# Optimization experiments

Measured on AMD Instinct MI355X. Metric: run time of the kernel, lower is better.

## Reference

```python
import jax, jax.numpy as jnp
import numpy as np

B, S, E, H = 8, 2048, 1024, 128  # batch, seq, emd_dim, head_size
DROP_P = 0.1


def setup_inputs() -> dict:
    key = jax.random.key(0)
    kx, ku, kq, kk, kv = jax.random.split(key, 5)
    x = jax.random.normal(kx, (B, S, E), dtype=jnp.float32)
    drop_u = jax.random.uniform(ku, (B, S, S), dtype=jnp.float32)
    # Linear(emd_dim, head_size, bias=False): store weights as [E, H] so y = x @ W
    scale = 1.0 / np.sqrt(E)
    wq = jax.random.uniform(kq, (E, H), dtype=jnp.float32, minval=-scale, maxval=scale)
    wk = jax.random.uniform(kk, (E, H), dtype=jnp.float32, minval=-scale, maxval=scale)
    wv = jax.random.uniform(kv, (E, H), dtype=jnp.float32, minval=-scale, maxval=scale)
    return {"x": x, "wq": wq, "wk": wk, "wv": wv, "drop_u": drop_u}


def reference(x, wq, wk, wv, drop_u):
    Edim = x.shape[-1]
    q = x @ wq  # [B,S,H]
    k = x @ wk
    v = x @ wv
    # NOTE: module scales by emd_dim**-0.5 (E), not head_size**-0.5
    att = jnp.einsum("bsh,bth->bst", q, k) * (Edim ** -0.5)
    att = jax.nn.softmax(att, axis=-1)
    # deterministic inverted dropout with p=0.1
    keep = (drop_u >= DROP_P).astype(att.dtype) / (1.0 - DROP_P)
    att = att * keep
    return jnp.einsum("bst,bth->bsh", att, v)
```

## Files before the change

kernel.cpp:

```cpp
#include <hip/hip_runtime.h>
#include <hip/hip_bf16.h>
#include <stdint.h>
#include <stddef.h>

#define B_ 8
#define S_ 2048
#define E_ 1024
#define H_ 128
#define NR_ (B_ * S_)

typedef __attribute__((ext_vector_type(8))) short short8;
typedef __attribute__((ext_vector_type(4))) float f32x4;

__device__ __forceinline__ short f2bf(float f){
  uint32_t u = __builtin_bit_cast(uint32_t, f);
  u = (u + 0x7FFFu + ((u >> 16) & 1u)) >> 16;
  return (short)(uint16_t)u;
}

#define GLOBAL_AS __attribute__((address_space(1)))
#define LDS_AS    __attribute__((address_space(3)))
__device__ __forceinline__ void async16(const void* g, void* l){
  __builtin_amdgcn_global_load_lds((const GLOBAL_AS uint32_t*)g,
                                   (LDS_AS uint32_t*)l, 16, 0, 0);
}

__global__ void pack_w(const float* __restrict__ wq, const float* __restrict__ wk,
                       const float* __restrict__ wv, short* __restrict__ wt){
  __shared__ float t[32][33];
  int idx = blockIdx.x;
  int hb  = idx & 3;
  int eb  = (idx >> 2) & 31;
  int w   = idx >> 7;
  const float* src = (w == 0) ? wq : (w == 1) ? wk : wv;
  int c  = threadIdx.x & 31;
  int r0 = threadIdx.x >> 5;
#pragma unroll
  for (int i = 0; i < 4; i++){
    int r = r0 * 4 + i;
    t[r][c] = src[(size_t)(eb * 32 + r) * H_ + hb * 32 + c];
  }
  __syncthreads();
#pragma unroll
  for (int i = 0; i < 4; i++){
    int r = r0 * 4 + i;
    wt[(size_t)(w * 128 + hb * 32 + r) * E_ + eb * 32 + c] = f2bf(t[c][r]);
  }
}

__launch_bounds__(256)
__global__ void qkv_gemm(const float* __restrict__ x, const short* __restrict__ wt,
                         short* __restrict__ qm, short* __restrict__ km,
                         short* __restrict__ vtmp){
  __shared__ __align__(16) short slab[2][12288];
  const int wave = threadIdx.x >> 6;
  const int lane = threadIdx.x & 63;
  const int l16  = lane & 15;
  const int quad = lane >> 4;
  const int m0   = blockIdx.x * 32;

  f32x4 acc[2][6];
#pragma unroll
  for (int a = 0; a < 2; a++)
#pragma unroll
    for (int b = 0; b < 6; b++) acc[a][b] = (f32x4)(0.0f);

  const float* xr0 = x + (size_t)(m0 + l16) * E_ + quad * 8;
  const float* xr1 = xr0 + (size_t)16 * E_;

#define STAGE(buf, k0)                                                        \
  {                                                                           \
    _Pragma("unroll")                                                         \
    for (int i = 0; i < 6; i++){                                              \
      int c  = wave * 6 + i;                                                  \
      int kc = c & 3;                                                         \
      int nb = c >> 2;                                                        \
      const short* gp = wt + (size_t)(nb * 64 + lane) * E_ + (k0) + kc * 8;   \
      async16(gp, (char*)slab[buf] + kc * 6144 + nb * 1024);                  \
    }                                                                         \
  }

  STAGE(0, 0)
  for (int ks = 0; ks < 32; ks++){
    const int k0 = ks * 32;
    __syncthreads();
    if (ks < 31) STAGE((ks + 1) & 1, k0 + 32)

    f32x4 a00 = *(const f32x4*)(xr0 + k0);
    f32x4 a01 = *(const f32x4*)(xr0 + k0 + 4);
    f32x4 a10 = *(const f32x4*)(xr1 + k0);
    f32x4 a11 = *(const f32x4*)(xr1 + k0 + 4);
    short8 af0, af1;
#pragma unroll
    for (int j = 0; j < 4; j++){
      af0[j] = f2bf(a00[j]); af0[j + 4] = f2bf(a01[j]);
      af1[j] = f2bf(a10[j]); af1[j + 4] = f2bf(a11[j]);
    }

    const char* sb = (const char*)slab[ks & 1];
#pragma unroll
    for (int j = 0; j < 6; j++){
      int nt = wave * 6 + j;
      short8 bf = *(const short8*)(sb + quad * 6144 + (size_t)(nt * 16 + l16) * 16);
      acc[0][j] = __builtin_amdgcn_mfma_f32_16x16x32_bf16(af0, bf, acc[0][j], 0, 0, 0);
      acc[1][j] = __builtin_amdgcn_mfma_f32_16x16x32_bf16(af1, bf, acc[1][j], 0, 0, 0);
    }
  }
#undef STAGE

#pragma unroll
  for (int mt = 0; mt < 2; mt++)
#pragma unroll
    for (int j = 0; j < 6; j++){
      int c0  = wave * 96 + j * 16;
      short* dst = (c0 < 128) ? qm : (c0 < 256) ? km : vtmp;
      int cin = c0 & 127;
      int row = m0 + mt * 16 + quad * 4;
#pragma unroll
      for (int r = 0; r < 4; r++)
        dst[(size_t)(row + r) * H_ + cin + l16] = f2bf(acc[mt][j][r]);
    }
}

__global__ void transpose_v(const short* __restrict__ v, short* __restrict__ vt){
  __shared__ short t[32][33];
  int idx = blockIdx.x;
  int hb = idx & 3;
  int sb = (idx >> 2) & 63;
  int b  = idx >> 8;
  int s0 = sb * 32, h0 = hb * 32;
  int c  = threadIdx.x & 31;
  int r0 = threadIdx.x >> 5;
#pragma unroll
  for (int i = 0; i < 4; i++){
    int r = r0 * 4 + i;
    t[r][c] = v[((size_t)b * S_ + s0 + r) * H_ + h0 + c];
  }
  __syncthreads();
#pragma unroll
  for (int i = 0; i < 4; i++){
    int r = r0 * 4 + i;
    vt[((size_t)b * H_ + h0 + r) * S_ + s0 + c] = t[c][r];
  }
}

__launch_bounds__(256)
__global__ void attn(const short* __restrict__ qm, const short* __restrict__ km,
                     const short* __restrict__ vtm, const float* __restrict__ du,
                     float* __restrict__ po, float* __restrict__ pl,
                     float* __restrict__ out, int split){
  const int wave = threadIdx.x >> 6;
  const int lane = threadIdx.x & 63;
  const int l16  = lane & 15;
  const int quad = lane >> 4;
  const int sp   = blockIdx.x & (split - 1);
  const int rbk  = blockIdx.x / split;
  const int b    = rbk >> 5;
  const int m0   = (rbk & 31) * 64 + wave * 16;
  const int seg  = S_ / split;

  const short* qb  = qm  + ((size_t)b * S_ + m0) * H_;
  const short* kb  = km  + (size_t)b * S_ * H_;
  const short* vb  = vtm + (size_t)b * H_ * S_;
  const float* dub = du  + ((size_t)b * S_ + m0) * S_;

  __shared__ __align__(16) short kls[8192];
  __shared__ __align__(16) short vls[8192];
  __shared__ float pbuf[4][16][68];
  float* pb = &pbuf[wave][0][0];

  short8 qf[4];
#pragma unroll
  for (int kc = 0; kc < 4; kc++)
    qf[kc] = *(const short8*)(qb + (size_t)l16 * H_ + kc * 32 + quad * 8);

  f32x4 o[8];
#pragma unroll
  for (int ht = 0; ht < 8; ht++) o[ht] = (f32x4)(0.0f);
  float lpart[4] = {0.f, 0.f, 0.f, 0.f};

  const float SC2  = 0.045084220f;
  const float KINV = 1.0f / 0.9f;

  const int tbeg = sp * seg;
  for (int t0 = tbeg; t0 < tbeg + seg; t0 += 64){
#pragma unroll
    for (int i = 0; i < 4; i++){
      int c = wave * 4 + i;
      int r = c * 4 + (lane >> 4);
      int s = lane & 15;
      int q = (s & 8) | ((s ^ r) & 7);
      async16(kb + (size_t)(t0 + r) * H_ + q * 8, (char*)kls + c * 1024);
    }
#pragma unroll
    for (int i = 0; i < 4; i++){
      int c = wave * 4 + i;
      int r = c * 8 + (lane >> 3);
      int s = lane & 7;
      int q = (s ^ r) & 7;
      async16(vb + (size_t)r * S_ + t0 + q * 8, (char*)vls + c * 1024);
    }
    __syncthreads();

    const float* dp = dub + (size_t)l16 * S_ + t0 + quad * 8;
    f32x4 u0 = *(const f32x4*)(dp);
    f32x4 u1 = *(const f32x4*)(dp + 4);
    f32x4 u2 = *(const f32x4*)(dp + 32);
    f32x4 u3 = *(const f32x4*)(dp + 36);

    f32x4 s[4];
#pragma unroll
    for (int nt = 0; nt < 4; nt++) s[nt] = (f32x4)(0.0f);
#pragma unroll
    for (int nt = 0; nt < 4; nt++){
      int row = nt * 16 + l16;
#pragma unroll
      for (int kc = 0; kc < 4; kc++){
        int q  = kc * 4 + quad;
        int ph = (q & 8) | ((q ^ row) & 7);
        short8 bf = *(const short8*)((const char*)kls + row * 256 + ph * 16);
        s[nt] = __builtin_amdgcn_mfma_f32_16x16x32_bf16(qf[kc], bf, s[nt], 0, 0, 0);
      }
    }

#pragma unroll
    for (int nt = 0; nt < 4; nt++)
#pragma unroll
      for (int r = 0; r < 4; r++){
        float p = exp2f(s[nt][r] * SC2);
        lpart[r] += p;
        pb[(quad * 4 + r) * 68 + nt * 16 + l16] = p;
      }

    __builtin_amdgcn_sched_barrier(0);
    __builtin_amdgcn_s_waitcnt(0xC07F);
    __builtin_amdgcn_sched_barrier(0);

    const float* pr = pb + l16 * 68 + quad * 8;
    f32x4 p0 = *(const f32x4*)(pr);
    f32x4 p1 = *(const f32x4*)(pr + 4);
    f32x4 p2 = *(const f32x4*)(pr + 32);
    f32x4 p3 = *(const f32x4*)(pr + 36);
    short8 pa0, pa1;
#pragma unroll
    for (int j = 0; j < 4; j++){
      pa0[j]     = f2bf((u0[j] >= 0.1f) ? p0[j] * KINV : 0.0f);
      pa0[j + 4] = f2bf((u1[j] >= 0.1f) ? p1[j] * KINV : 0.0f);
      pa1[j]     = f2bf((u2[j] >= 0.1f) ? p2[j] * KINV : 0.0f);
      pa1[j + 4] = f2bf((u3[j] >= 0.1f) ? p3[j] * KINV : 0.0f);
    }

#pragma unroll
    for (int ht = 0; ht < 8; ht++){
      int row = ht * 16 + l16;
#pragma unroll
      for (int half = 0; half < 2; half++){
        int q  = half * 4 + quad;
        int ph = (q ^ row) & 7;
        short8 vf = *(const short8*)((const char*)vls + row * 128 + ph * 16);
        o[ht] = __builtin_amdgcn_mfma_f32_16x16x32_bf16(half ? pa1 : pa0, vf, o[ht], 0, 0, 0);
      }
    }
    __syncthreads();
  }

  float lrow[4];
#pragma unroll
  for (int r = 0; r < 4; r++){
    float v = lpart[r];
    v += __shfl_xor(v, 1);
    v += __shfl_xor(v, 2);
    v += __shfl_xor(v, 4);
    v += __shfl_xor(v, 8);
    lrow[r] = v;
  }

  if (split == 1){
    float* op = out + ((size_t)b * S_ + m0) * H_;
#pragma unroll
    for (int ht = 0; ht < 8; ht++)
#pragma unroll
      for (int r = 0; r < 4; r++)
        op[(size_t)(quad * 4 + r) * H_ + ht * 16 + l16] = o[ht][r] / lrow[r];
  } else {
#pragma unroll
    for (int r = 0; r < 4; r++){
      size_t R = (size_t)b * S_ + m0 + quad * 4 + r;
#pragma unroll
      for (int ht = 0; ht < 8; ht++)
        po[((size_t)sp * NR_ + R) * H_ + ht * 16 + l16] = o[ht][r];
      if (l16 == 0) pl[(size_t)sp * NR_ + R] = lrow[r];
    }
  }
}

__global__ void combine(const float* __restrict__ po, const float* __restrict__ pl,
                        float* __restrict__ out, int split){
  int row = blockIdx.x;
  int col = threadIdx.x;
  float num = 0.f, den = 0.f;
  for (int s = 0; s < split; s++){
    num += po[((size_t)s * NR_ + row) * H_ + col];
    den += pl[(size_t)s * NR_ + row];
  }
  out[(size_t)row * H_ + col] = num / den;
}

extern "C" void kernel_launch(void* const* d_in, const int* in_sizes, int n_in,
                              void* d_out, int out_size, void* d_ws, size_t ws_size,
                              hipStream_t stream){
  const float* x  = (const float*)d_in[0];
  const float* wq = (const float*)d_in[1];
  const float* wk = (const float*)d_in[2];
  const float* wv = (const float*)d_in[3];
  const float* du = (const float*)d_in[4];
  float* out = (float*)d_out;

  const size_t MiB = 1048576;
  char* ws = (char*)d_ws;
  short* qm  = (short*)(ws);
  short* km  = (short*)(ws + 4 * MiB);
  short* vt  = (short*)(ws + 8 * MiB);
  float* pl  = (float*)(ws + 12 * MiB);
  float* po  = (float*)(ws + 12 * MiB + 524288);
  short* wt   = (short*)(ws + 12 * MiB + 524288);
  short* vtmp = (short*)(ws + 12 * MiB + 524288 + 1 * MiB);

  size_t base  = 12 * MiB + 524288;
  size_t need4 = base + 4 * 8 * MiB;
  size_t need2 = base + 2 * 8 * MiB;
  int split = (ws_size >= need4) ? 4 : (ws_size >= need2) ? 2 : 1;

  hipLaunchKernelGGL(pack_w,      dim3(384),  dim3(256), 0, stream, wq, wk, wv, wt);
  hipLaunchKernelGGL(qkv_gemm,    dim3(512),  dim3(256), 0, stream, x, wt, qm, km, vtmp);
  hipLaunchKernelGGL(transpose_v, dim3(2048), dim3(256), 0, stream, vtmp, vt);
  hipLaunchKernelGGL(attn, dim3(256 * split), dim3(256), 0, stream,
                     qm, km, vt, du, po, pl, out, split);
  if (split > 1)
    hipLaunchKernelGGL(combine, dim3(NR_), dim3(H_), 0, stream, po, pl, out, split);
}
```

Baseline: 360.2 us.

## Pre-cast x to bf16 and retile QKV GEMM into 128x128 LDS-staged tiles

Adds a separate kernel that casts x to bf16 once. The QKV projection is restructured into 128x128 output tiles over a 3x128 grid. Both A and B operands are staged into swizzled LDS through async global-to-LDS loads, and each wave computes a 4x4 block of MFMA tiles. This removes the per-block fp32 loads and conversions of x and improves operand reuse, at the cost of an extra pass writing and reading x in bf16 and a more complex workspace layout.

```diff
diff --git a/kernel.cpp b/kernel.cpp
--- a/kernel.cpp
+++ b/kernel.cpp
@@ -23,6 +23,16 @@
 __device__ __forceinline__ void async16(const void* g, void* l){
   __builtin_amdgcn_global_load_lds((const GLOBAL_AS uint32_t*)g,
                                    (LDS_AS uint32_t*)l, 16, 0, 0);
+}
+
+__global__ void cast_x(const float* __restrict__ x, short* __restrict__ xb){
+  size_t i = ((size_t)blockIdx.x * 256 + threadIdx.x) * 8;
+  f32x4 a = *(const f32x4*)(x + i);
+  f32x4 b = *(const f32x4*)(x + i + 4);
+  short8 o;
+#pragma unroll
+  for (int j = 0; j < 4; j++){ o[j] = f2bf(a[j]); o[j + 4] = f2bf(b[j]); }
+  *(short8*)(xb + i) = o;
 }
 
 __global__ void pack_w(const float* __restrict__ wq, const float* __restrict__ wk,
@@ -49,34 +59,36 @@
 }
 
 __launch_bounds__(256)
-__global__ void qkv_gemm(const float* __restrict__ x, const short* __restrict__ wt,
+__global__ void qkv_gemm(const short* __restrict__ xb, const short* __restrict__ wt,
                          short* __restrict__ qm, short* __restrict__ km,
                          short* __restrict__ vtmp){
-  __shared__ __align__(16) short slab[2][12288];
+  __shared__ __align__(16) short abuf[2][4096];
+  __shared__ __align__(16) short bbuf[2][4096];
   const int wave = threadIdx.x >> 6;
   const int lane = threadIdx.x & 63;
   const int l16  = lane & 15;
   const int quad = lane >> 4;
-  const int m0   = blockIdx.x * 32;
-
-  f32x4 acc[2][6];
-#pragma unroll
-  for (int a = 0; a < 2; a++)
-#pragma unroll
-    for (int b = 0; b < 6; b++) acc[a][b] = (f32x4)(0.0f);
-
-  const float* xr0 = x + (size_t)(m0 + l16) * E_ + quad * 8;
-  const float* xr1 = xr0 + (size_t)16 * E_;
+  const int nb   = blockIdx.x;
+  const int m0   = blockIdx.y * 128;
+  const int n0   = nb * 128;
+
+  f32x4 acc[4][4];
+#pragma unroll
+  for (int i = 0; i < 4; i++)
+#pragma unroll
+    for (int j = 0; j < 4; j++) acc[i][j] = (f32x4)(0.0f);
 
 #define STAGE(buf, k0)                                                        \
   {                                                                           \
     _Pragma("unroll")                                                         \
-    for (int i = 0; i < 6; i++){                                              \
-      int c  = wave * 6 + i;                                                  \
-      int kc = c & 3;                                                         \
-      int nb = c >> 2;                                                        \
-      const short* gp = wt + (size_t)(nb * 64 + lane) * E_ + (k0) + kc * 8;   \
-      async16(gp, (char*)slab[buf] + kc * 6144 + nb * 1024);                  \
+    for (int i = 0; i < 2; i++){                                              \
+      int c = wave * 2 + i;                                                   \
+      int r = c * 16 + (lane >> 2);                                           \
+      int q = ((lane & 3) ^ ((r >> 1) & 3)) & 3;                              \
+      async16(xb + (size_t)(m0 + r) * E_ + (k0) + q * 8,                      \
+              (char*)abuf[buf] + c * 1024);                                   \
+      async16(wt + (size_t)(n0 + r) * E_ + (k0) + q * 8,                      \
+              (char*)bbuf[buf] + c * 1024);                                   \
     }                                                                         \
   }
 
@@ -86,39 +98,36 @@
     __syncthreads();
     if (ks < 31) STAGE((ks + 1) & 1, k0 + 32)
 
-    f32x4 a00 = *(const f32x4*)(xr0 + k0);
-    f32x4 a01 = *(const f32x4*)(xr0 + k0 + 4);
-    f32x4 a10 = *(const f32x4*)(xr1 + k0);
-    f32x4 a11 = *(const f32x4*)(xr1 + k0 + 4);
-    short8 af0, af1;
-#pragma unroll
-    for (int j = 0; j < 4; j++){
-      af0[j] = f2bf(a00[j]); af0[j + 4] = f2bf(a01[j]);
-      af1[j] = f2bf(a10[j]); af1[j + 4] = f2bf(a11[j]);
-    }
-
-    const char* sb = (const char*)slab[ks & 1];
-#pragma unroll
-    for (int j = 0; j < 6; j++){
-      int nt = wave * 6 + j;
-      short8 bf = *(const short8*)(sb + quad * 6144 + (size_t)(nt * 16 + l16) * 16);
-      acc[0][j] = __builtin_amdgcn_mfma_f32_16x16x32_bf16(af0, bf, acc[0][j], 0, 0, 0);
-      acc[1][j] = __builtin_amdgcn_mfma_f32_16x16x32_bf16(af1, bf, acc[1][j], 0, 0, 0);
-    }
+    const short* ab = abuf[ks & 1];
+    const short* bb = bbuf[ks & 1];
+    short8 af[4], bf[4];
+#pragma unroll
+    for (int t = 0; t < 4; t++){
+      int ra = (wave & 1) * 64 + t * 16 + l16;
+      int pa = (quad ^ ((ra >> 1) & 3)) & 3;
+      af[t] = *(const short8*)(ab + ra * 32 + pa * 8);
+      int rb = (wave >> 1) * 64 + t * 16 + l16;
+      int pb = (quad ^ ((rb >> 1) & 3)) & 3;
+      bf[t] = *(const short8*)(bb + rb * 32 + pb * 8);
+    }
+#pragma unroll
+    for (int mt = 0; mt < 4; mt++)
+#pragma unroll
+      for (int nt = 0; nt < 4; nt++)
+        acc[mt][nt] = __builtin_amdgcn_mfma_f32_16x16x32_bf16(af[mt], bf[nt], acc[mt][nt], 0, 0, 0);
   }
 #undef STAGE
 
-#pragma unroll
-  for (int mt = 0; mt < 2; mt++)
-#pragma unroll
-    for (int j = 0; j < 6; j++){
-      int c0  = wave * 96 + j * 16;
-      short* dst = (c0 < 128) ? qm : (c0 < 256) ? km : vtmp;
-      int cin = c0 & 127;
-      int row = m0 + mt * 16 + quad * 4;
+  short* dst = (nb == 0) ? qm : (nb == 1) ? km : vtmp;
+#pragma unroll
+  for (int mt = 0; mt < 4; mt++)
+#pragma unroll
+    for (int nt = 0; nt < 4; nt++){
+      int row = m0 + (wave & 1) * 64 + mt * 16 + quad * 4;
+      int col = (wave >> 1) * 64 + nt * 16 + l16;
 #pragma unroll
       for (int r = 0; r < 4; r++)
-        dst[(size_t)(row + r) * H_ + cin + l16] = f2bf(acc[mt][j][r]);
+        dst[(size_t)(row + r) * H_ + col] = f2bf(acc[mt][nt][r]);
     }
 }
 
@@ -318,23 +327,41 @@
 
   const size_t MiB = 1048576;
   char* ws = (char*)d_ws;
-  short* qm  = (short*)(ws);
-  short* km  = (short*)(ws + 4 * MiB);
-  short* vt  = (short*)(ws + 8 * MiB);
-  float* pl  = (float*)(ws + 12 * MiB);
-  float* po  = (float*)(ws + 12 * MiB + 524288);
-  short* wt   = (short*)(ws + 12 * MiB + 524288);
-  short* vtmp = (short*)(ws + 12 * MiB + 524288 + 1 * MiB);
-
-  size_t base  = 12 * MiB + 524288;
-  size_t need4 = base + 4 * 8 * MiB;
-  size_t need2 = base + 2 * 8 * MiB;
-  int split = (ws_size >= need4) ? 4 : (ws_size >= need2) ? 2 : 1;
-
-  hipLaunchKernelGGL(pack_w,      dim3(384),  dim3(256), 0, stream, wq, wk, wv, wt);
-  hipLaunchKernelGGL(qkv_gemm,    dim3(512),  dim3(256), 0, stream, x, wt, qm, km, vtmp);
-  hipLaunchKernelGGL(transpose_v, dim3(2048), dim3(256), 0, stream, vtmp, vt);
-  hipLaunchKernelGGL(attn, dim3(256 * split), dim3(256), 0, stream,
+  short* qm = (short*)(ws);
+  short* km = (short*)(ws + 4 * MiB);
+  short* vt = (short*)(ws + 8 * MiB);
+
+  size_t needA = (size_t)(76.5 * MiB);
+  size_t needB = (size_t)(60.5 * MiB);
+  int split;
+  float *pl = nullptr, *po = nullptr;
+  short *wt, *vtmp, *xb;
+  if (ws_size >= needA){
+    split = 4;
+    pl   = (float*)(ws + 12 * MiB);
+    po   = (float*)(ws + 12 * MiB + 524288);
+    wt   = (short*)(ws + 12 * MiB + 524288);
+    vtmp = (short*)(ws + 12 * MiB + 524288 + 1 * MiB);
+    xb   = (short*)(ws + 12 * MiB + 524288 + 32 * MiB);
+  } else if (ws_size >= needB){
+    split = 2;
+    pl   = (float*)(ws + 12 * MiB);
+    po   = (float*)(ws + 12 * MiB + 524288);
+    wt   = (short*)(ws + 12 * MiB + 524288);
+    vtmp = (short*)(ws + 12 * MiB + 524288 + 1 * MiB);
+    xb   = (short*)(ws + 12 * MiB + 524288 + 16 * MiB);
+  } else {
+    split = 1;
+    xb   = (short*)(ws + 8 * MiB);
+    wt   = (short*)(ws + 40 * MiB);
+    vtmp = (short*)(ws + 40 * MiB + 786432);
+  }
+
+  hipLaunchKernelGGL(cast_x,      dim3(8192),      dim3(256), 0, stream, x, xb);
+  hipLaunchKernelGGL(pack_w,      dim3(384),       dim3(256), 0, stream, wq, wk, wv, wt);
+  hipLaunchKernelGGL(qkv_gemm,    dim3(3, 128),    dim3(256), 0, stream, xb, wt, qm, km, vtmp);
+  hipLaunchKernelGGL(transpose_v, dim3(2048),      dim3(256), 0, stream, vtmp, vt);
+  hipLaunchKernelGGL(attn,        dim3(256 * split), dim3(256), 0, stream,
                      qm, km, vt, du, po, pl, out, split);
   if (split > 1)
     hipLaunchKernelGGL(combine, dim3(NR_), dim3(H_), 0, stream, po, pl, out, split);
```

Result: faster. 302.1 us (-16.1%).
